# Performance work log

Hardware: AMD Instinct MI355X
Metric: run time of the kernel (lower is better)

Reference implementation:

```python
import jax, jax.numpy as jnp
import numpy as np

N_NODES = 10000
N_EDGES = 160000
D_IN = 512
D_OUT = 512


def setup_inputs() -> dict:
    key = jax.random.key(0)
    k_x, k_e, k_wl, k_wr = jax.random.split(key, 4)
    x = jax.random.normal(k_x, (N_NODES, D_IN), dtype=jnp.float32)
    edge_index = jax.random.randint(k_e, (2, N_EDGES), 0, N_NODES, dtype=jnp.int64)
    scale = 1.0 / np.sqrt(D_IN)
    W_l = jax.random.normal(k_wl, (D_IN, D_OUT), dtype=jnp.float32) * scale
    W_r = jax.random.normal(k_wr, (D_IN, D_OUT), dtype=jnp.float32) * scale
    b = jnp.zeros((D_OUT,), dtype=jnp.float32)
    return {"x": x, "edge_index": edge_index, "W_l": W_l, "W_r": W_r, "b": b}


def reference(x, edge_index, W_l, W_r, b):
    # dropout p=0.0 -> identity
    src = edge_index[0]  # message sources (x_j)
    dst = edge_index[1]  # aggregation targets (i)
    n = x.shape[0]
    # mean neighbor aggregation: scatter-add messages, divide by in-degree
    msg = x[src]                                   # [E, D_in]
    agg = jax.ops.segment_sum(msg, dst, num_segments=n)        # [N, D_in]
    deg = jax.ops.segment_sum(jnp.ones((src.shape[0],), x.dtype), dst, num_segments=n)
    mean = agg / jnp.maximum(deg, 1.0)[:, None]
    # SAGEConv: lin_l(aggregated) + lin_r(root), bias in lin_l
    h = mean @ W_l + b + x @ W_r                   # [N, D_out]
    # Swish activation
    return h * jax.nn.sigmoid(h)
```

## Files before the change

### kernel.cpp

```cpp
#include <hip/hip_runtime.h>
#include <cstdint>
#include <cstddef>

typedef unsigned short ushort_t;
typedef __attribute__((ext_vector_type(8))) short short8;
typedef __attribute__((ext_vector_type(4))) float float4_;
typedef __attribute__((ext_vector_type(2))) float float2_;

#define GLOBAL_AS __attribute__((address_space(1)))
#define LDS_AS    __attribute__((address_space(3)))

#define D_FEAT 512
#define KDIM   1024
#define CAP    80
#define BK     128

__device__ __forceinline__ ushort_t f2bf(float f) {
    union { float f; unsigned int i; } v; v.f = f;
    unsigned int x = v.i;
    unsigned int r = (x + 0x7fffu + ((x >> 16) & 1u)) >> 16;
    return (ushort_t)r;
}

__device__ __forceinline__ void accq(float* acc, uint2 v) {
    float2_ a01 = __builtin_amdgcn_cvt_pk_f32_fp8(v.x, false);
    float2_ a23 = __builtin_amdgcn_cvt_pk_f32_fp8(v.x, true);
    float2_ a45 = __builtin_amdgcn_cvt_pk_f32_fp8(v.y, false);
    float2_ a67 = __builtin_amdgcn_cvt_pk_f32_fp8(v.y, true);
    acc[0] += a01.x; acc[1] += a01.y;
    acc[2] += a23.x; acc[3] += a23.y;
    acc[4] += a45.x; acc[5] += a45.y;
    acc[6] += a67.x; acc[7] += a67.y;
}

__global__ __launch_bounds__(256) void prep_kernel(
    const float* __restrict__ Wl, const float* __restrict__ Wr,
    const float* __restrict__ x, const int* __restrict__ ei,
    ushort_t* __restrict__ BT, ushort_t* __restrict__ xb,
    unsigned char* __restrict__ xq, unsigned int* __restrict__ cnt,
    int* __restrict__ colbuf, int N, int E, int nchunks, int cb) {
    int b = blockIdx.x;
    int t = threadIdx.x;
    if (b < cb) {
        int idx = b * 256 + t;
        if (idx >= nchunks) return;
        int row = idx >> 7;
        int c = (idx & 127) << 2;
        float4 v = *(const float4*)&x[(size_t)row * D_FEAT + c];
        ushort_t o[4] = {f2bf(v.x), f2bf(v.y), f2bf(v.z), f2bf(v.w)};
        *(uint2*)&xb[(size_t)row * D_FEAT + c] = *(const uint2*)o;
        int pk = 0;
        pk = __builtin_amdgcn_cvt_pk_fp8_f32(v.x, v.y, pk, false);
        pk = __builtin_amdgcn_cvt_pk_fp8_f32(v.z, v.w, pk, true);
        *(int*)&xq[(size_t)row * D_FEAT + c] = pk;
    } else if (b < cb + 128) {
        int bb = b - cb;
        __shared__ float tile[64][68];
        int kb = (bb & 15) * 64, nb = (bb >> 4) * 64;
#pragma unroll
        for (int ph = 0; ph < 4; ++ph) {
            int f = t * 4 + ph * 1024;
            int k = f >> 6, n = f & 63;
            int gk = kb + k;
            const float* W = (gk < 512) ? (Wl + (size_t)gk * 512 + nb + n)
                                        : (Wr + (size_t)(gk - 512) * 512 + nb + n);
            *(float4*)&tile[k][n] = *(const float4*)W;
        }
        __syncthreads();
#pragma unroll
        for (int ph = 0; ph < 4; ++ph) {
            int f = t * 4 + ph * 1024;
            int n = f >> 6, k = f & 63;
            ushort_t tmp[4];
#pragma unroll
            for (int j = 0; j < 4; ++j) tmp[j] = f2bf(tile[k + j][n]);
            *(uint2*)&BT[(size_t)(nb + n) * KDIM + kb + k] = *(const uint2*)tmp;
        }
    } else {
        int e = ((b - cb - 128) * 256 + t) * 2;
        if (e >= E) return;
        unsigned int V = cnt[N];
        int2 d2 = *(const int2*)&ei[E + e];
        int2 s2 = *(const int2*)&ei[e];
        unsigned int p0 = atomicAdd(&cnt[d2.x], 1u) - V;
        if (p0 < CAP) colbuf[(size_t)d2.x * CAP + p0] = s2.x;
        if (e + 1 < E) {
            unsigned int p1 = atomicAdd(&cnt[d2.y], 1u) - V;
            if (p1 < CAP) colbuf[(size_t)d2.y * CAP + p1] = s2.y;
        }
    }
}

__global__ __launch_bounds__(256) void agg_kernel(
    const unsigned char* __restrict__ xq, ushort_t* __restrict__ mb,
    const unsigned int* __restrict__ cnt, const int* __restrict__ colbuf,
    int n) {
    int w = threadIdx.x >> 6, l = threadIdx.x & 63;
    int node = blockIdx.x * 4 + w;
    if (node >= n) return;
    unsigned int V = cnt[n];
    int f = l << 3;
    const unsigned char* gsrc = xq + f;
    const int* bucket = colbuf + (size_t)node * CAP;
    float acc[8] = {0.f, 0.f, 0.f, 0.f, 0.f, 0.f, 0.f, 0.f};
    int deg = (int)(cnt[node] - V);
    int e = deg < CAP ? deg : CAP;
    int j = 0;
    for (; j + 7 < e; j += 8) {
        int4 i0 = *(const int4*)&bucket[j];
        int4 i1 = *(const int4*)&bucket[j + 4];
        uint2 v0 = *(const uint2*)(gsrc + (size_t)i0.x * D_FEAT);
        uint2 v1 = *(const uint2*)(gsrc + (size_t)i0.y * D_FEAT);
        uint2 v2 = *(const uint2*)(gsrc + (size_t)i0.z * D_FEAT);
        uint2 v3 = *(const uint2*)(gsrc + (size_t)i0.w * D_FEAT);
        uint2 v4 = *(const uint2*)(gsrc + (size_t)i1.x * D_FEAT);
        uint2 v5 = *(const uint2*)(gsrc + (size_t)i1.y * D_FEAT);
        uint2 v6 = *(const uint2*)(gsrc + (size_t)i1.z * D_FEAT);
        uint2 v7 = *(const uint2*)(gsrc + (size_t)i1.w * D_FEAT);
        accq(acc, v0); accq(acc, v1); accq(acc, v2); accq(acc, v3);
        accq(acc, v4); accq(acc, v5); accq(acc, v6); accq(acc, v7);
    }
    if (j + 3 < e) {
        int4 i0 = *(const int4*)&bucket[j];
        uint2 v0 = *(const uint2*)(gsrc + (size_t)i0.x * D_FEAT);
        uint2 v1 = *(const uint2*)(gsrc + (size_t)i0.y * D_FEAT);
        uint2 v2 = *(const uint2*)(gsrc + (size_t)i0.z * D_FEAT);
        uint2 v3 = *(const uint2*)(gsrc + (size_t)i0.w * D_FEAT);
        accq(acc, v0); accq(acc, v1); accq(acc, v2); accq(acc, v3);
        j += 4;
    }
    for (; j < e; ++j) {
        uint2 v0 = *(const uint2*)(gsrc + (size_t)bucket[j] * D_FEAT);
        accq(acc, v0);
    }
    float scale = 1.0f / (float)(deg > 1 ? deg : 1);
    ushort_t o[8];
#pragma unroll
    for (int k = 0; k < 8; ++k) o[k] = f2bf(acc[k] * scale);
    *(uint4*)&mb[(size_t)node * D_FEAT + f] = *(const uint4*)o;
}

__global__ __launch_bounds__(256) void gemm_kernel(
    const ushort_t* __restrict__ mb, const ushort_t* __restrict__ xb,
    const ushort_t* __restrict__ BT, const float* __restrict__ bias,
    float* __restrict__ out, int nrows) {
    __shared__ ushort_t As[64 * BK];
    __shared__ ushort_t Bs[64 * BK];
    int b = blockIdx.x;
    int sg = b >> 6, local = b & 63;
    int tile_m = (sg * 8 + (local & 7)) * 64;
    int tile_n = (local >> 3) * 64;
    int tid = threadIdx.x;
    int l = tid & 63;
    int w = tid >> 6;
    int lm = l & 15, q = l >> 4;
    int wm = (w >> 1) * 32, wn = (w & 1) * 32;

    float4_ acc[2][2];
#pragma unroll
    for (int i = 0; i < 2; ++i)
#pragma unroll
        for (int j = 0; j < 2; ++j) acc[i][j] = (float4_)(0.f);

    for (int k0 = 0; k0 < KDIM; k0 += BK) {
        const ushort_t* Asrc = (k0 < 512) ? mb : xb;
        int kk = k0 & 511;
#pragma unroll
        for (int cc = 0; cc < 4; ++cc) {
            int c = tid + cc * 256;
            int row = c >> 4;
            int kc = (c & 15) ^ (row & 15);
            const ushort_t* gp =
                Asrc + (size_t)(tile_m + row) * D_FEAT + kk + kc * 8;
            __builtin_amdgcn_global_load_lds(
                (const GLOBAL_AS unsigned int*)gp,
                (LDS_AS unsigned int*)&As[c * 8], 16, 0, 0);
            const ushort_t* gq =
                BT + (size_t)(tile_n + row) * KDIM + k0 + kc * 8;
            __builtin_amdgcn_global_load_lds(
                (const GLOBAL_AS unsigned int*)gq,
                (LDS_AS unsigned int*)&Bs[c * 8], 16, 0, 0);
        }
        __syncthreads();

#pragma unroll
        for (int s = 0; s < 4; ++s) {
            int kc = s * 4 + q;
            short8 a[2], bb[2];
#pragma unroll
            for (int i = 0; i < 2; ++i) {
                int row = wm + i * 16 + lm;
                a[i] = *(const short8*)&As[row * BK + ((kc ^ (row & 15)) << 3)];
            }
#pragma unroll
            for (int j = 0; j < 2; ++j) {
                int col = wn + j * 16 + lm;
                bb[j] = *(const short8*)&Bs[col * BK + ((kc ^ (col & 15)) << 3)];
            }
#pragma unroll
            for (int i = 0; i < 2; ++i)
#pragma unroll
                for (int j = 0; j < 2; ++j)
                    acc[i][j] = __builtin_amdgcn_mfma_f32_16x16x32_bf16(
                        a[i], bb[j], acc[i][j], 0, 0, 0);
        }
        __syncthreads();
    }

#pragma unroll
    for (int j = 0; j < 2; ++j) {
        int gcol = tile_n + wn + j * 16 + lm;
        float bv = bias[gcol];
#pragma unroll
        for (int i = 0; i < 2; ++i) {
#pragma unroll
            for (int r = 0; r < 4; ++r) {
                int grow = tile_m + wm + i * 16 + q * 4 + r;
                if (grow < nrows) {
                    float h = acc[i][j][r] + bv;
                    float sw = h / (1.f + __expf(-h));
                    out[(size_t)grow * D_FEAT + gcol] = sw;
                }
            }
        }
    }
}

extern "C" void kernel_launch(void* const* d_in, const int* in_sizes, int n_in,
                              void* d_out, int out_size, void* d_ws, size_t ws_size,
                              hipStream_t stream) {
    const float* x    = (const float*)d_in[0];
    const int*   ei   = (const int*)d_in[1];
    const float* Wl   = (const float*)d_in[2];
    const float* Wr   = (const float*)d_in[3];
    const float* bias = (const float*)d_in[4];
    float* out = (float*)d_out;

    const int N = in_sizes[0] / D_FEAT;
    const int E = in_sizes[1] / 2;
    int mt = (N + 63) / 64;
    mt = (mt + 7) & ~7;
    const int M_PAD = mt * 64;

    char* ws = (char*)d_ws;
    size_t off = 0;
    auto take = [&](size_t bytes) -> char* {
        char* p = ws + off;
        off += (bytes + 255) & ~(size_t)255;
        return p;
    };
    ushort_t*      xb     = (ushort_t*)take((size_t)M_PAD * D_FEAT * 2);
    ushort_t*      mb     = (ushort_t*)take((size_t)M_PAD * D_FEAT * 2);
    ushort_t*      BT     = (ushort_t*)take((size_t)D_FEAT * KDIM * 2);
    unsigned char* xq     = (unsigned char*)take((size_t)M_PAD * D_FEAT);
    unsigned int*  cnt    = (unsigned int*)take((size_t)M_PAD * 4);
    int*           colbuf = (int*)take((size_t)M_PAD * CAP * 4);

    int nchunks = N * (D_FEAT / 4);
    int cb = (nchunks + 255) / 256;
    int eb = (E / 2 + 255) / 256;
    prep_kernel<<<cb + 128 + eb, 256, 0, stream>>>(
        Wl, Wr, x, ei, BT, xb, xq, cnt, colbuf, N, E, nchunks, cb);

    agg_kernel<<<(N + 3) / 4, 256, 0, stream>>>(xq, mb, cnt, colbuf, N);

    gemm_kernel<<<mt * 8, 256, 0, stream>>>(mb, xb, BT, bias, out, N);
}
```

Baseline: 128.1 us.

## Widen aggregation gathers to 16 bytes and merge A operands into one buffer

The aggregation kernel now has each wavefront split into two halves that process alternate neighbors. Each lane gathers 16 fp8 features with a single 16-byte load, and the two halves are combined with a cross-half shuffle. The mean and bf16 copies of x are now written into one concatenated [M, 1024] A matrix, so the GEMM loads from a single contiguous source with no per-k-step pointer selection. This is meant to cut the number of gather instructions and improve memory-level parallelism, at the cost of more accumulator registers and a shuffle reduction.

```diff
diff --git a/kernel.cpp b/kernel.cpp
--- a/kernel.cpp
+++ b/kernel.cpp
@@ -22,21 +22,22 @@
     return (ushort_t)r;
 }
 
-__device__ __forceinline__ void accq(float* acc, uint2 v) {
-    float2_ a01 = __builtin_amdgcn_cvt_pk_f32_fp8(v.x, false);
-    float2_ a23 = __builtin_amdgcn_cvt_pk_f32_fp8(v.x, true);
-    float2_ a45 = __builtin_amdgcn_cvt_pk_f32_fp8(v.y, false);
-    float2_ a67 = __builtin_amdgcn_cvt_pk_f32_fp8(v.y, true);
-    acc[0] += a01.x; acc[1] += a01.y;
-    acc[2] += a23.x; acc[3] += a23.y;
-    acc[4] += a45.x; acc[5] += a45.y;
-    acc[6] += a67.x; acc[7] += a67.y;
+__device__ __forceinline__ void acc16(float* acc, uint4 v) {
+    float2_ a;
+    a = __builtin_amdgcn_cvt_pk_f32_fp8(v.x, false); acc[0] += a.x;  acc[1] += a.y;
+    a = __builtin_amdgcn_cvt_pk_f32_fp8(v.x, true);  acc[2] += a.x;  acc[3] += a.y;
+    a = __builtin_amdgcn_cvt_pk_f32_fp8(v.y, false); acc[4] += a.x;  acc[5] += a.y;
+    a = __builtin_amdgcn_cvt_pk_f32_fp8(v.y, true);  acc[6] += a.x;  acc[7] += a.y;
+    a = __builtin_amdgcn_cvt_pk_f32_fp8(v.z, false); acc[8] += a.x;  acc[9] += a.y;
+    a = __builtin_amdgcn_cvt_pk_f32_fp8(v.z, true);  acc[10] += a.x; acc[11] += a.y;
+    a = __builtin_amdgcn_cvt_pk_f32_fp8(v.w, false); acc[12] += a.x; acc[13] += a.y;
+    a = __builtin_amdgcn_cvt_pk_f32_fp8(v.w, true);  acc[14] += a.x; acc[15] += a.y;
 }
 
 __global__ __launch_bounds__(256) void prep_kernel(
     const float* __restrict__ Wl, const float* __restrict__ Wr,
     const float* __restrict__ x, const int* __restrict__ ei,
-    ushort_t* __restrict__ BT, ushort_t* __restrict__ xb,
+    ushort_t* __restrict__ BT, ushort_t* __restrict__ Ab,
     unsigned char* __restrict__ xq, unsigned int* __restrict__ cnt,
     int* __restrict__ colbuf, int N, int E, int nchunks, int cb) {
     int b = blockIdx.x;
@@ -48,7 +49,7 @@
         int c = (idx & 127) << 2;
         float4 v = *(const float4*)&x[(size_t)row * D_FEAT + c];
         ushort_t o[4] = {f2bf(v.x), f2bf(v.y), f2bf(v.z), f2bf(v.w)};
-        *(uint2*)&xb[(size_t)row * D_FEAT + c] = *(const uint2*)o;
+        *(uint2*)&Ab[(size_t)row * KDIM + D_FEAT + c] = *(const uint2*)o;
         int pk = 0;
         pk = __builtin_amdgcn_cvt_pk_fp8_f32(v.x, v.y, pk, false);
         pk = __builtin_amdgcn_cvt_pk_fp8_f32(v.z, v.w, pk, true);
@@ -92,58 +93,59 @@
 }
 
 __global__ __launch_bounds__(256) void agg_kernel(
-    const unsigned char* __restrict__ xq, ushort_t* __restrict__ mb,
+    const unsigned char* __restrict__ xq, ushort_t* __restrict__ Ab,
     const unsigned int* __restrict__ cnt, const int* __restrict__ colbuf,
     int n) {
     int w = threadIdx.x >> 6, l = threadIdx.x & 63;
     int node = blockIdx.x * 4 + w;
     if (node >= n) return;
     unsigned int V = cnt[n];
-    int f = l << 3;
-    const unsigned char* gsrc = xq + f;
+    int half = l >> 5, sub = l & 31;
+    const unsigned char* gsrc = xq + sub * 16;
     const int* bucket = colbuf + (size_t)node * CAP;
-    float acc[8] = {0.f, 0.f, 0.f, 0.f, 0.f, 0.f, 0.f, 0.f};
+    float acc[16];
+#pragma unroll
+    for (int k = 0; k < 16; ++k) acc[k] = 0.f;
     int deg = (int)(cnt[node] - V);
     int e = deg < CAP ? deg : CAP;
     int j = 0;
     for (; j + 7 < e; j += 8) {
-        int4 i0 = *(const int4*)&bucket[j];
-        int4 i1 = *(const int4*)&bucket[j + 4];
-        uint2 v0 = *(const uint2*)(gsrc + (size_t)i0.x * D_FEAT);
-        uint2 v1 = *(const uint2*)(gsrc + (size_t)i0.y * D_FEAT);
-        uint2 v2 = *(const uint2*)(gsrc + (size_t)i0.z * D_FEAT);
-        uint2 v3 = *(const uint2*)(gsrc + (size_t)i0.w * D_FEAT);
-        uint2 v4 = *(const uint2*)(gsrc + (size_t)i1.x * D_FEAT);
-        uint2 v5 = *(const uint2*)(gsrc + (size_t)i1.y * D_FEAT);
-        uint2 v6 = *(const uint2*)(gsrc + (size_t)i1.z * D_FEAT);
-        uint2 v7 = *(const uint2*)(gsrc + (size_t)i1.w * D_FEAT);
-        accq(acc, v0); accq(acc, v1); accq(acc, v2); accq(acc, v3);
-        accq(acc, v4); accq(acc, v5); accq(acc, v6); accq(acc, v7);
-    }
-    if (j + 3 < e) {
-        int4 i0 = *(const int4*)&bucket[j];
-        uint2 v0 = *(const uint2*)(gsrc + (size_t)i0.x * D_FEAT);
-        uint2 v1 = *(const uint2*)(gsrc + (size_t)i0.y * D_FEAT);
-        uint2 v2 = *(const uint2*)(gsrc + (size_t)i0.z * D_FEAT);
-        uint2 v3 = *(const uint2*)(gsrc + (size_t)i0.w * D_FEAT);
-        accq(acc, v0); accq(acc, v1); accq(acc, v2); accq(acc, v3);
-        j += 4;
-    }
-    for (; j < e; ++j) {
-        uint2 v0 = *(const uint2*)(gsrc + (size_t)bucket[j] * D_FEAT);
-        accq(acc, v0);
-    }
-    float scale = 1.0f / (float)(deg > 1 ? deg : 1);
-    ushort_t o[8];
-#pragma unroll
-    for (int k = 0; k < 8; ++k) o[k] = f2bf(acc[k] * scale);
-    *(uint4*)&mb[(size_t)node * D_FEAT + f] = *(const uint4*)o;
+        int s0 = bucket[j + half];
+        int s1 = bucket[j + 2 + half];
+        int s2 = bucket[j + 4 + half];
+        int s3 = bucket[j + 6 + half];
+        uint4 v0 = *(const uint4*)(gsrc + (size_t)s0 * D_FEAT);
+        uint4 v1 = *(const uint4*)(gsrc + (size_t)s1 * D_FEAT);
+        uint4 v2 = *(const uint4*)(gsrc + (size_t)s2 * D_FEAT);
+        uint4 v3 = *(const uint4*)(gsrc + (size_t)s3 * D_FEAT);
+        acc16(acc, v0); acc16(acc, v1); acc16(acc, v2); acc16(acc, v3);
+    }
+    for (; j + 1 < e; j += 2) {
+        int s0 = bucket[j + half];
+        uint4 v0 = *(const uint4*)(gsrc + (size_t)s0 * D_FEAT);
+        acc16(acc, v0);
+    }
+    if (j < e && half == 0) {
+        int s0 = bucket[j];
+        uint4 v0 = *(const uint4*)(gsrc + (size_t)s0 * D_FEAT);
+        acc16(acc, v0);
+    }
+#pragma unroll
+    for (int k = 0; k < 16; ++k) acc[k] += __shfl_xor(acc[k], 32);
+    if (half == 0) {
+        float scale = 1.0f / (float)(deg > 1 ? deg : 1);
+        ushort_t o[16];
+#pragma unroll
+        for (int k = 0; k < 16; ++k) o[k] = f2bf(acc[k] * scale);
+        ushort_t* dst = Ab + (size_t)node * KDIM + sub * 16;
+        *(uint4*)dst = *(const uint4*)&o[0];
+        *(uint4*)(dst + 8) = *(const uint4*)&o[8];
+    }
 }
 
 __global__ __launch_bounds__(256) void gemm_kernel(
-    const ushort_t* __restrict__ mb, const ushort_t* __restrict__ xb,
-    const ushort_t* __restrict__ BT, const float* __restrict__ bias,
-    float* __restrict__ out, int nrows) {
+    const ushort_t* __restrict__ Ab, const ushort_t* __restrict__ BT,
+    const float* __restrict__ bias, float* __restrict__ out, int nrows) {
     __shared__ ushort_t As[64 * BK];
     __shared__ ushort_t Bs[64 * BK];
     int b = blockIdx.x;
@@ -163,15 +165,13 @@
         for (int j = 0; j < 2; ++j) acc[i][j] = (float4_)(0.f);
 
     for (int k0 = 0; k0 < KDIM; k0 += BK) {
-        const ushort_t* Asrc = (k0 < 512) ? mb : xb;
-        int kk = k0 & 511;
 #pragma unroll
         for (int cc = 0; cc < 4; ++cc) {
             int c = tid + cc * 256;
             int row = c >> 4;
             int kc = (c & 15) ^ (row & 15);
             const ushort_t* gp =
-                Asrc + (size_t)(tile_m + row) * D_FEAT + kk + kc * 8;
+                Ab + (size_t)(tile_m + row) * KDIM + k0 + kc * 8;
             __builtin_amdgcn_global_load_lds(
                 (const GLOBAL_AS unsigned int*)gp,
                 (LDS_AS unsigned int*)&As[c * 8], 16, 0, 0);
@@ -249,8 +249,7 @@
         off += (bytes + 255) & ~(size_t)255;
         return p;
     };
-    ushort_t*      xb     = (ushort_t*)take((size_t)M_PAD * D_FEAT * 2);
-    ushort_t*      mb     = (ushort_t*)take((size_t)M_PAD * D_FEAT * 2);
+    ushort_t*      Ab     = (ushort_t*)take((size_t)M_PAD * KDIM * 2);
     ushort_t*      BT     = (ushort_t*)take((size_t)D_FEAT * KDIM * 2);
     unsigned char* xq     = (unsigned char*)take((size_t)M_PAD * D_FEAT);
     unsigned int*  cnt    = (unsigned int*)take((size_t)M_PAD * 4);
@@ -260,9 +259,9 @@
     int cb = (nchunks + 255) / 256;
     int eb = (E / 2 + 255) / 256;
     prep_kernel<<<cb + 128 + eb, 256, 0, stream>>>(
-        Wl, Wr, x, ei, BT, xb, xq, cnt, colbuf, N, E, nchunks, cb);
-
-    agg_kernel<<<(N + 3) / 4, 256, 0, stream>>>(xq, mb, cnt, colbuf, N);
-
-    gemm_kernel<<<mt * 8, 256, 0, stream>>>(mb, xb, BT, bias, out, N);
-}
+        Wl, Wr, x, ei, BT, Ab, xq, cnt, colbuf, N, E, nchunks, cb);
+
+    agg_kernel<<<(N + 3) / 4, 256, 0, stream>>>(xq, Ab, cnt, colbuf, N);
+
+    gemm_kernel<<<mt * 8, 256, 0, stream>>>(Ab, BT, bias, out, N);
+}
```

Result: no change. 129.7 us (+1.2%).
